# Performance work log

Measured on AMD Instinct MI355X. Metric: run time of the kernel, lower is better.

Reference implementation:

```python
import jax, jax.numpy as jnp
import numpy as np

RADIUS = 0.1      # ball-query radius; also max_dist in collision_error
THRESH = 0.001    # collision threshold
NSAMPLE = 4       # neighbors per query point
EPS = 1e-7
LOSS_WEIGHT = 1.0


def _face_normals(verts, faces):
    # verts: (b, n_v, 3), faces: (b, n_f, 3) int -> unit face normals (b, n_f, 3)
    tri = jax.vmap(lambda V, F: V[F])(verts, faces)  # (b, n_f, 3verts, 3xyz)
    e1 = tri[:, :, 1] - tri[:, :, 0]
    e2 = tri[:, :, 2] - tri[:, :, 0]
    fn = jnp.cross(e1, e2)
    return fn / (jnp.linalg.norm(fn, axis=-1, keepdims=True) + EPS)


def _vertex_normals(faces, fn, n_v):
    # sparse v2f bmm equivalent: average incident face normals per vertex
    def scatter(F, N):
        idx = F.reshape(-1)                    # (3*n_f,) face->vertex ids
        vals = jnp.repeat(N, 3, axis=0)        # each face normal to its 3 verts
        s = jnp.zeros((n_v, 3), N.dtype).at[idx].add(vals)
        c = jnp.zeros((n_v, 1), N.dtype).at[idx].add(jnp.float32(1.0))
        return s / (c + EPS)
    return jax.vmap(scatter)(faces, fn)        # (b, n_v, 3)


def _ball_query(new_xyz, xyz, radius, nsample):
    # PointNet++ ball query: first `nsample` points of xyz within radius of each
    # new_xyz point; unfilled slots repeat the first hit (0 if no hits).
    d2 = jnp.sum((new_xyz[:, :, None, :] - xyz[:, None, :, :]) ** 2, axis=-1)  # (b, nq, nv)
    within = d2 < radius * radius
    c = jnp.cumsum(within.astype(jnp.int32), axis=-1)
    n_within = c[..., -1]
    first_idx = jnp.argmax(within, axis=-1)    # 0 when no hits (matches CUDA kernel)
    slots = []
    for j in range(nsample):
        idx_j = jnp.argmax(within & (c == j + 1), axis=-1)
        slots.append(jnp.where(n_within > j, idx_j, first_idx))
    return jnp.stack(slots, axis=-1)           # (b, nq, nsample)


def _collision_loss(pred, h_state, h_faces):
    faces = jnp.swapaxes(h_faces, 1, 2)                 # (b, n_f, 3)
    human_verts = jnp.swapaxes(h_state, 1, 2)[..., :3]  # (b, n_v, 3)
    n_v = human_verts.shape[1]

    fn = _face_normals(human_verts, faces)
    vn = _vertex_normals(faces, fn, n_v)                # (b, n_v, 3)

    idx = _ball_query(pred, human_verts, RADIUS, NSAMPLE)      # (b, nq, K)
    gxyz = jax.vmap(lambda V, I: V[I])(human_verts, idx)       # (b, nq, K, 3)
    gn = jax.vmap(lambda V, I: V[I])(vn, idx)                  # (b, nq, K, 3)

    diff = pred[:, :, None, :] - gxyz
    gn = gn / (jnp.linalg.norm(gn, axis=-1, keepdims=True) + EPS)
    dot = jnp.sum(diff * gn, axis=-1)                   # (b, nq, K)
    valid_dot = (dot - THRESH) * (dot >= -RADIUS)       # max_dist = radius
    mask = valid_dot < 0
    per_pt = jnp.sum(valid_dot * mask / (jnp.sum(mask, axis=-1, keepdims=True) + EPS), axis=-1) ** 2
    avg_mask = per_pt > 0
    loss = jnp.sum(per_pt)                              # reduction='sum', weight=None
    loss = loss / (jnp.sum(avg_mask) + EPS)
    return LOSS_WEIGHT * loss


def setup_inputs() -> dict:
    key = jax.random.key(0)
    k1, k2, k3, k4 = jax.random.split(key, 4)
    bs, n_pred, n_v, n_f, C = 2, 8192, 6890, 13776, 6
    pred = jax.random.uniform(k1, (bs, n_pred, 3), dtype=jnp.float32)
    label = jax.random.uniform(k2, (bs, n_pred, 3), dtype=jnp.float32)
    h_state = jax.random.uniform(k3, (bs, C, n_v), dtype=jnp.float32)
    h_faces = jax.random.randint(k4, (bs, 3, n_f), 0, n_v, dtype=jnp.int32)
    return {"pred": pred, "label": label, "h_state": h_state, "h_faces": h_faces}


def reference(pred, label, h_state, h_faces):
    # label is unused by collision_error (kept for signature fidelity)
    return _collision_loss(pred, h_state, h_faces)
```

## Files before the change

### kernel.cpp

```cpp
#include <hip/hip_runtime.h>
#include <cstdint>
#include <climits>

#define EPSF 1e-7f
#define NCELL 1000
#define RPAD 0.10002f

__device__ __forceinline__ int cell_of(float x, float y, float z) {
    int cx = min(max((int)(x * 10.0f), 0), 9);
    int cy = min(max((int)(y * 10.0f), 0), 9);
    int cz = min(max((int)(z * 10.0f), 0), 9);
    return (cx * 10 + cy) * 10 + cz;
}

__global__ void k1_face_count(const float* __restrict__ hs,
                              const int* __restrict__ hf,
                              float* __restrict__ svec,
                              float* __restrict__ scnt,
                              int* __restrict__ counts,
                              int n_v, int n_f, int bs) {
    int t = blockIdx.x * blockDim.x + threadIdx.x;
    if (t < bs * n_f) {
        int b = t / n_f;
        int f = t - b * n_f;
        const int* fb = hf + (size_t)b * 3 * n_f;
        int i0 = fb[f];
        int i1 = fb[n_f + f];
        int i2 = fb[2 * n_f + f];
        const float* xs = hs + (size_t)b * 6 * n_v;
        const float* ys = xs + n_v;
        const float* zs = xs + 2 * n_v;
        float ax = xs[i0], ay = ys[i0], az = zs[i0];
        float bx = xs[i1], by = ys[i1], bz = zs[i1];
        float cx = xs[i2], cy = ys[i2], cz = zs[i2];
        float e1x = bx - ax, e1y = by - ay, e1z = bz - az;
        float e2x = cx - ax, e2y = cy - ay, e2z = cz - az;
        float fx = e1y * e2z - e1z * e2y;
        float fy = e1z * e2x - e1x * e2z;
        float fz = e1x * e2y - e1y * e2x;
        float nrm = sqrtf(fx * fx + fy * fy + fz * fz) + EPSF;
        fx /= nrm; fy /= nrm; fz /= nrm;
        float* sb = svec + (size_t)b * n_v * 3;
        float* cb = scnt + (size_t)b * n_v;
        int idx3[3] = {i0, i1, i2};
        #pragma unroll
        for (int k = 0; k < 3; ++k) {
            int i = idx3[k];
            atomicAdd(&sb[i * 3 + 0], fx);
            atomicAdd(&sb[i * 3 + 1], fy);
            atomicAdd(&sb[i * 3 + 2], fz);
            atomicAdd(&cb[i], 1.0f);
        }
    }
    if (t < bs * n_v) {
        int b = t / n_v;
        int v = t - b * n_v;
        const float* xs = hs + (size_t)b * 6 * n_v;
        float x = xs[v], y = xs[n_v + v], z = xs[2 * n_v + v];
        atomicAdd(&counts[b * NCELL + cell_of(x, y, z)], 1);
    }
}

__global__ void k2_vn_scan(float* __restrict__ svec,
                           const float* __restrict__ scnt,
                           const int* __restrict__ counts,
                           int* __restrict__ cellstart,
                           int* __restrict__ cursor,
                           int total_v, int nvb) {
    if (blockIdx.x < (unsigned)nvb) {
        int t = blockIdx.x * blockDim.x + threadIdx.x;
        if (t >= total_v) return;
        float cc = scnt[t] + EPSF;
        float vx = svec[t * 3 + 0] / cc;
        float vy = svec[t * 3 + 1] / cc;
        float vz = svec[t * 3 + 2] / cc;
        float nrm = sqrtf(vx * vx + vy * vy + vz * vz) + EPSF;
        svec[t * 3 + 0] = vx / nrm;
        svec[t * 3 + 1] = vy / nrm;
        svec[t * 3 + 2] = vz / nrm;
        return;
    }
    if (threadIdx.x >= 128) return;
    int batch = threadIdx.x >> 6;
    int lane = threadIdx.x & 63;
    int local[16];
    int mysum = 0;
    #pragma unroll
    for (int k = 0; k < 16; ++k) {
        int c = lane * 16 + k;
        int v = (c < NCELL) ? counts[batch * NCELL + c] : 0;
        local[k] = v;
        mysum += v;
    }
    int s = mysum;
    #pragma unroll
    for (int off = 1; off < 64; off <<= 1) {
        int n = __shfl_up(s, off);
        if (lane >= off) s += n;
    }
    int excl = s - mysum;
    #pragma unroll
    for (int k = 0; k < 16; ++k) {
        int c = lane * 16 + k;
        if (c < NCELL) {
            cellstart[batch * (NCELL + 1) + c] = excl;
            cursor[batch * NCELL + c] = excl;
            excl += local[k];
        }
    }
    if (lane == 63) cellstart[batch * (NCELL + 1) + NCELL] = s;
}

__global__ void k3_scatter(const float* __restrict__ hs,
                           int* __restrict__ cursor,
                           float4* __restrict__ spk,
                           int n_v, int bs) {
    int t = blockIdx.x * blockDim.x + threadIdx.x;
    if (t >= bs * n_v) return;
    int b = t / n_v;
    int v = t - b * n_v;
    const float* xs = hs + (size_t)b * 6 * n_v;
    float x = xs[v], y = xs[n_v + v], z = xs[2 * n_v + v];
    int cell = cell_of(x, y, z);
    int pos = atomicAdd(&cursor[b * NCELL + cell], 1);
    spk[(size_t)b * n_v + pos] = make_float4(x, y, z, __int_as_float(v));
}

__global__ void k4_query(const float* __restrict__ pred,
                         const float* __restrict__ hs,
                         const float* __restrict__ un,
                         const float4* __restrict__ spk,
                         const int* __restrict__ cellstart,
                         double* __restrict__ partial,
                         float* __restrict__ pcnt,
                         int n_v, int n_pred, int bs) {
    const int lane = threadIdx.x & 63;
    const int wave = threadIdx.x >> 6;
    const int wid = blockIdx.x * 4 + wave;
    const int nq = bs * n_pred;

    float per_pt = 0.0f;
    float is_pos = 0.0f;

    if (wid < nq) {
        const int b = wid / n_pred;
        const float* xs = hs + (size_t)b * 6 * n_v;
        const float* ys = xs + n_v;
        const float* zs = xs + 2 * n_v;
        const float* unb = un + (size_t)b * n_v * 3;
        const float4* sp = spk + (size_t)b * n_v;
        const int* csb = cellstart + b * (NCELL + 1);
        const float px = pred[(size_t)wid * 3 + 0];
        const float py = pred[(size_t)wid * 3 + 1];
        const float pz = pred[(size_t)wid * 3 + 2];

        int xlo = max(0, (int)floorf((px - RPAD) * 10.0f));
        int xhi = min(9, (int)floorf((px + RPAD) * 10.0f));
        int ylo = max(0, (int)floorf((py - RPAD) * 10.0f));
        int yhi = min(9, (int)floorf((py + RPAD) * 10.0f));
        int zlo = max(0, (int)floorf((pz - RPAD) * 10.0f));
        int zhi = min(9, (int)floorf((pz + RPAD) * 10.0f));

        int rs[9], re[9];
        #pragma unroll
        for (int i = 0; i < 9; ++i) {
            int cx = xlo + i / 3;
            int cy = ylo + i % 3;
            bool valid = (cx <= xhi) && (cy <= yhi);
            int rowbase = (min(cx, 9) * 10 + min(cy, 9)) * 10;
            int lo = csb[rowbase + zlo];
            int hi = csb[rowbase + zhi + 1];
            rs[i] = valid ? lo : 0;
            re[i] = valid ? hi : 0;
        }

        int l0 = INT_MAX, l1 = INT_MAX, l2 = INT_MAX, l3 = INT_MAX;
        #pragma unroll
        for (int i = 0; i < 9; ++i) {
            for (int p = rs[i] + lane; p < re[i]; p += 64) {
                float4 c4 = sp[p];
                float dx = px - c4.x;
                float dy = py - c4.y;
                float dz = pz - c4.z;
                float d2 = dx * dx + dy * dy + dz * dz;
                if (d2 < 0.01f) {
                    int vid = __float_as_int(c4.w);
                    if (vid < l3) {
                        if (vid < l1) {
                            if (vid < l0) { l3 = l2; l2 = l1; l1 = l0; l0 = vid; }
                            else          { l3 = l2; l2 = l1; l1 = vid; }
                        } else {
                            if (vid < l2) { l3 = l2; l2 = vid; }
                            else          { l3 = vid; }
                        }
                    }
                }
            }
        }

        int a0 = l0, a1 = l1, a2 = l2, a3 = l3;
        int s0, s1, s2, s3;
        #pragma unroll
        for (int j = 0; j < 4; ++j) {
            int m = a0;
            #pragma unroll
            for (int off = 1; off < 64; off <<= 1) m = min(m, __shfl_xor(m, off));
            if (j == 0) s0 = m; else if (j == 1) s1 = m; else if (j == 2) s2 = m; else s3 = m;
            if (a0 == m && m != INT_MAX) { a0 = a1; a1 = a2; a2 = a3; a3 = INT_MAX; }
        }
        int id0 = (s0 == INT_MAX) ? 0 : s0;
        int id1 = (s1 == INT_MAX) ? id0 : s1;
        int id2 = (s2 == INT_MAX) ? id0 : s2;
        int id3 = (s3 == INT_MAX) ? id0 : s3;
        int ids[4] = {id0, id1, id2, id3};

        float vd[4];
        float cm = 0.0f;
        #pragma unroll
        for (int j = 0; j < 4; ++j) {
            int id = ids[j];
            float dx = px - xs[id];
            float dy = py - ys[id];
            float dz = pz - zs[id];
            float nx = unb[id * 3 + 0];
            float ny = unb[id * 3 + 1];
            float nz = unb[id * 3 + 2];
            float dot = dx * nx + dy * ny + dz * nz;
            float w = (dot >= -0.1f) ? 1.0f : 0.0f;
            float v = (dot - 0.001f) * w;
            bool msk = v < 0.0f;
            vd[j] = msk ? v : 0.0f;
            cm += msk ? 1.0f : 0.0f;
        }
        float s = ((vd[0] + vd[1]) + vd[2]) + vd[3];
        float a = s / (cm + EPSF);
        per_pt = a * a;
        is_pos = (per_pt > 0.0f) ? 1.0f : 0.0f;
    }

    __shared__ float ls[4];
    __shared__ float lc[4];
    if (lane == 0) { ls[wave] = per_pt; lc[wave] = is_pos; }
    __syncthreads();
    if (threadIdx.x == 0) {
        partial[blockIdx.x] = (double)ls[0] + (double)ls[1] + (double)ls[2] + (double)ls[3];
        pcnt[blockIdx.x] = ((lc[0] + lc[1]) + lc[2]) + lc[3];
    }
}

__global__ void finalize_kernel(const double* __restrict__ partial,
                                const float* __restrict__ pcnt,
                                int n, float* __restrict__ out) {
    double s = 0.0, c = 0.0;
    for (int i = threadIdx.x; i < n; i += blockDim.x) {
        s += partial[i];
        c += (double)pcnt[i];
    }
    #pragma unroll
    for (int off = 32; off > 0; off >>= 1) {
        s += __shfl_down(s, off);
        c += __shfl_down(c, off);
    }
    __shared__ double ws_s[4];
    __shared__ double ws_c[4];
    int wave = threadIdx.x >> 6;
    int lane = threadIdx.x & 63;
    if (lane == 0) { ws_s[wave] = s; ws_c[wave] = c; }
    __syncthreads();
    if (threadIdx.x == 0) {
        double S = ws_s[0] + ws_s[1] + ws_s[2] + ws_s[3];
        double C = ws_c[0] + ws_c[1] + ws_c[2] + ws_c[3];
        out[0] = (float)(S / (C + 1e-7));
    }
}

extern "C" void kernel_launch(void* const* d_in, const int* in_sizes, int n_in,
                              void* d_out, int out_size, void* d_ws, size_t ws_size,
                              hipStream_t stream) {
    const float* pred    = (const float*)d_in[0];
    const float* h_state = (const float*)d_in[2];
    const int*   h_faces = (const int*)d_in[3];
    float* out = (float*)d_out;

    const int bs = 2;
    const int n_pred = in_sizes[0] / (bs * 3);
    const int n_v    = in_sizes[2] / (bs * 6);
    const int n_f    = in_sizes[3] / (bs * 3);
    const int nq = bs * n_pred;
    const int nblk = (nq + 3) / 4;

    size_t o_svec    = 0;
    size_t o_scnt    = o_svec + (size_t)bs * n_v * 3;
    size_t o_counts  = o_scnt + (size_t)bs * n_v;
    size_t o_zeroend = (o_counts + (size_t)bs * NCELL + 3) & ~(size_t)3;
    size_t o_cursor  = o_zeroend;
    size_t o_cs      = o_cursor + (size_t)bs * NCELL;
    size_t o_partial = (o_cs + (size_t)bs * (NCELL + 1) + 1) & ~(size_t)1;
    size_t o_pcnt    = o_partial + 2 * (size_t)nblk;
    size_t o_spk     = (o_pcnt + (size_t)nblk + 3) & ~(size_t)3;

    float* base = (float*)d_ws;
    float*  svec      = base + o_svec;
    float*  scnt      = base + o_scnt;
    int*    counts    = (int*)(base + o_counts);
    int*    cursor    = (int*)(base + o_cursor);
    int*    cellstart = (int*)(base + o_cs);
    double* partial   = (double*)(base + o_partial);
    float*  pcnt      = base + o_pcnt;
    float4* spk       = (float4*)(base + o_spk);

    hipMemsetAsync(d_ws, 0, o_zeroend * sizeof(float), stream);

    int t1 = bs * n_f;
    k1_face_count<<<(t1 + 255) / 256, 256, 0, stream>>>(
        h_state, h_faces, svec, scnt, counts, n_v, n_f, bs);

    int nvb = (bs * n_v + 255) / 256;
    k2_vn_scan<<<nvb + 1, 256, 0, stream>>>(
        svec, scnt, counts, cellstart, cursor, bs * n_v, nvb);

    k3_scatter<<<(bs * n_v + 255) / 256, 256, 0, stream>>>(
        h_state, cursor, spk, n_v, bs);

    k4_query<<<nblk, 256, 0, stream>>>(
        pred, h_state, svec, spk, cellstart, partial, pcnt,
        n_v, n_pred, bs);

    finalize_kernel<<<1, 256, 0, stream>>>(partial, pcnt, nblk, out);
}
```

Baseline: 111.2 us.

## Fuse scan and scatter into one kernel, flatten cell loop, pack vertex data

The prefix scan and the vertex scatter are merged into one kernel that uses a shared-memory cursor per batch, and one launch is dropped. The query kernel flattens its nine per-row cell loops into a single index space and prefetches up to six float4 groups before computing distances, to raise memory-level parallelism. The four rounds of wave min-reduction are replaced by a butterfly merge of sorted top-4 lists. Vertex positions and normals are packed as float4 pairs for the final gather. The scatter now runs on only one block per batch, which serialises that work, and the fixed candidate prefetch buffer raises register pressure.

```diff
diff --git a/kernel.cpp b/kernel.cpp
--- a/kernel.cpp
+++ b/kernel.cpp
@@ -5,6 +5,7 @@
 #define EPSF 1e-7f
 #define NCELL 1000
 #define RPAD 0.10002f
+#define MAXG 6
 
 __device__ __forceinline__ int cell_of(float x, float y, float z) {
     int cx = min(max((int)(x * 10.0f), 0), 9);
@@ -61,74 +62,73 @@
     }
 }
 
-__global__ void k2_vn_scan(float* __restrict__ svec,
-                           const float* __restrict__ scnt,
-                           const int* __restrict__ counts,
-                           int* __restrict__ cellstart,
-                           int* __restrict__ cursor,
-                           int total_v, int nvb) {
+__global__ void k2_build(const float* __restrict__ hs,
+                         const float* __restrict__ svec,
+                         const float* __restrict__ scnt,
+                         const int* __restrict__ counts,
+                         int* __restrict__ cellstart,
+                         float4* __restrict__ vert,
+                         float4* __restrict__ spk,
+                         int n_v, int bs, int nvb) {
+    __shared__ int cursor_l[NCELL];
     if (blockIdx.x < (unsigned)nvb) {
         int t = blockIdx.x * blockDim.x + threadIdx.x;
-        if (t >= total_v) return;
+        if (t >= bs * n_v) return;
+        int b = t / n_v;
+        int v = t - b * n_v;
         float cc = scnt[t] + EPSF;
         float vx = svec[t * 3 + 0] / cc;
         float vy = svec[t * 3 + 1] / cc;
         float vz = svec[t * 3 + 2] / cc;
         float nrm = sqrtf(vx * vx + vy * vy + vz * vz) + EPSF;
-        svec[t * 3 + 0] = vx / nrm;
-        svec[t * 3 + 1] = vy / nrm;
-        svec[t * 3 + 2] = vz / nrm;
+        const float* xs = hs + (size_t)b * 6 * n_v;
+        float x = xs[v], y = xs[n_v + v], z = xs[2 * n_v + v];
+        vert[2 * (size_t)t + 0] = make_float4(x, y, z, 0.0f);
+        vert[2 * (size_t)t + 1] = make_float4(vx / nrm, vy / nrm, vz / nrm, 0.0f);
         return;
     }
-    if (threadIdx.x >= 128) return;
-    int batch = threadIdx.x >> 6;
-    int lane = threadIdx.x & 63;
-    int local[16];
-    int mysum = 0;
-    #pragma unroll
-    for (int k = 0; k < 16; ++k) {
-        int c = lane * 16 + k;
-        int v = (c < NCELL) ? counts[batch * NCELL + c] : 0;
-        local[k] = v;
-        mysum += v;
-    }
-    int s = mysum;
-    #pragma unroll
-    for (int off = 1; off < 64; off <<= 1) {
-        int n = __shfl_up(s, off);
-        if (lane >= off) s += n;
-    }
-    int excl = s - mysum;
-    #pragma unroll
-    for (int k = 0; k < 16; ++k) {
-        int c = lane * 16 + k;
-        if (c < NCELL) {
-            cellstart[batch * (NCELL + 1) + c] = excl;
-            cursor[batch * NCELL + c] = excl;
-            excl += local[k];
-        }
-    }
-    if (lane == 63) cellstart[batch * (NCELL + 1) + NCELL] = s;
-}
-
-__global__ void k3_scatter(const float* __restrict__ hs,
-                           int* __restrict__ cursor,
-                           float4* __restrict__ spk,
-                           int n_v, int bs) {
-    int t = blockIdx.x * blockDim.x + threadIdx.x;
-    if (t >= bs * n_v) return;
-    int b = t / n_v;
-    int v = t - b * n_v;
-    const float* xs = hs + (size_t)b * 6 * n_v;
-    float x = xs[v], y = xs[n_v + v], z = xs[2 * n_v + v];
-    int cell = cell_of(x, y, z);
-    int pos = atomicAdd(&cursor[b * NCELL + cell], 1);
-    spk[(size_t)b * n_v + pos] = make_float4(x, y, z, __int_as_float(v));
-}
-
-__global__ void k4_query(const float* __restrict__ pred,
-                         const float* __restrict__ hs,
-                         const float* __restrict__ un,
+    int batch = blockIdx.x - nvb;
+    if (threadIdx.x < 64) {
+        int lane = threadIdx.x;
+        int local[16];
+        int mysum = 0;
+        #pragma unroll
+        for (int k = 0; k < 16; ++k) {
+            int c = lane * 16 + k;
+            int v = (c < NCELL) ? counts[batch * NCELL + c] : 0;
+            local[k] = v;
+            mysum += v;
+        }
+        int s = mysum;
+        #pragma unroll
+        for (int off = 1; off < 64; off <<= 1) {
+            int n = __shfl_up(s, off);
+            if (lane >= off) s += n;
+        }
+        int excl = s - mysum;
+        #pragma unroll
+        for (int k = 0; k < 16; ++k) {
+            int c = lane * 16 + k;
+            if (c < NCELL) {
+                cellstart[batch * (NCELL + 1) + c] = excl;
+                cursor_l[c] = excl;
+                excl += local[k];
+            }
+        }
+        if (lane == 63) cellstart[batch * (NCELL + 1) + NCELL] = s;
+    }
+    __syncthreads();
+    const float* xs = hs + (size_t)batch * 6 * n_v;
+    for (int v = threadIdx.x; v < n_v; v += blockDim.x) {
+        float x = xs[v], y = xs[n_v + v], z = xs[2 * n_v + v];
+        int cell = cell_of(x, y, z);
+        int pos = atomicAdd(&cursor_l[cell], 1);
+        spk[(size_t)batch * n_v + pos] = make_float4(x, y, z, __int_as_float(v));
+    }
+}
+
+__global__ void k3_query(const float* __restrict__ pred,
+                         const float4* __restrict__ vert,
                          const float4* __restrict__ spk,
                          const int* __restrict__ cellstart,
                          double* __restrict__ partial,
@@ -144,10 +144,7 @@
 
     if (wid < nq) {
         const int b = wid / n_pred;
-        const float* xs = hs + (size_t)b * 6 * n_v;
-        const float* ys = xs + n_v;
-        const float* zs = xs + 2 * n_v;
-        const float* unb = un + (size_t)b * n_v * 3;
+        const float4* vb = vert + 2 * (size_t)b * n_v;
         const float4* sp = spk + (size_t)b * n_v;
         const int* csb = cellstart + b * (NCELL + 1);
         const float px = pred[(size_t)wid * 3 + 0];
@@ -173,12 +170,61 @@
             rs[i] = valid ? lo : 0;
             re[i] = valid ? hi : 0;
         }
+        int B[10];
+        B[0] = 0;
+        #pragma unroll
+        for (int i = 0; i < 9; ++i) B[i + 1] = B[i] + (re[i] - rs[i]);
+        const int T = B[9];
+        int D[9];
+        #pragma unroll
+        for (int i = 0; i < 9; ++i) D[i] = rs[i] - B[i];
 
         int l0 = INT_MAX, l1 = INT_MAX, l2 = INT_MAX, l3 = INT_MAX;
-        #pragma unroll
-        for (int i = 0; i < 9; ++i) {
-            for (int p = rs[i] + lane; p < re[i]; p += 64) {
-                float4 c4 = sp[p];
+
+        if (T > 0) {
+            float4 cbuf[MAXG];
+            #pragma unroll
+            for (int g = 0; g < MAXG; ++g) {
+                if (g * 64 < T) {
+                    int pc = min(g * 64 + lane, T - 1);
+                    int addr = pc + D[0];
+                    #pragma unroll
+                    for (int i = 1; i < 9; ++i)
+                        addr = (pc >= B[i]) ? pc + D[i] : addr;
+                    cbuf[g] = sp[addr];
+                }
+            }
+            #pragma unroll
+            for (int g = 0; g < MAXG; ++g) {
+                if (g * 64 < T) {
+                    int p = g * 64 + lane;
+                    if (p < T) {
+                        float4 c4 = cbuf[g];
+                        float dx = px - c4.x;
+                        float dy = py - c4.y;
+                        float dz = pz - c4.z;
+                        float d2 = dx * dx + dy * dy + dz * dz;
+                        if (d2 < 0.01f) {
+                            int vid = __float_as_int(c4.w);
+                            if (vid < l3) {
+                                if (vid < l1) {
+                                    if (vid < l0) { l3 = l2; l2 = l1; l1 = l0; l0 = vid; }
+                                    else          { l3 = l2; l2 = l1; l1 = vid; }
+                                } else {
+                                    if (vid < l2) { l3 = l2; l2 = vid; }
+                                    else          { l3 = vid; }
+                                }
+                            }
+                        }
+                    }
+                }
+            }
+            for (int p = MAXG * 64 + lane; p < T; p += 64) {
+                int addr = p + D[0];
+                #pragma unroll
+                for (int i = 1; i < 9; ++i)
+                    addr = (p >= B[i]) ? p + D[i] : addr;
+                float4 c4 = sp[addr];
                 float dx = px - c4.x;
                 float dy = py - c4.y;
                 float dz = pz - c4.z;
@@ -198,20 +244,26 @@
             }
         }
 
-        int a0 = l0, a1 = l1, a2 = l2, a3 = l3;
-        int s0, s1, s2, s3;
-        #pragma unroll
-        for (int j = 0; j < 4; ++j) {
-            int m = a0;
-            #pragma unroll
-            for (int off = 1; off < 64; off <<= 1) m = min(m, __shfl_xor(m, off));
-            if (j == 0) s0 = m; else if (j == 1) s1 = m; else if (j == 2) s2 = m; else s3 = m;
-            if (a0 == m && m != INT_MAX) { a0 = a1; a1 = a2; a2 = a3; a3 = INT_MAX; }
-        }
-        int id0 = (s0 == INT_MAX) ? 0 : s0;
-        int id1 = (s1 == INT_MAX) ? id0 : s1;
-        int id2 = (s2 == INT_MAX) ? id0 : s2;
-        int id3 = (s3 == INT_MAX) ? id0 : s3;
+        #pragma unroll
+        for (int off = 1; off < 64; off <<= 1) {
+            int r0 = __shfl_xor(l3, off);
+            int r1 = __shfl_xor(l2, off);
+            int r2 = __shfl_xor(l1, off);
+            int r3 = __shfl_xor(l0, off);
+            int m0 = min(l0, r0);
+            int m1 = min(l1, r1);
+            int m2 = min(l2, r2);
+            int m3 = min(l3, r3);
+            int t0 = min(m0, m2), t2 = max(m0, m2);
+            int t1 = min(m1, m3), t3 = max(m1, m3);
+            l0 = min(t0, t1); l1 = max(t0, t1);
+            l2 = min(t2, t3); l3 = max(t2, t3);
+        }
+
+        int id0 = (l0 == INT_MAX) ? 0 : l0;
+        int id1 = (l1 == INT_MAX) ? id0 : l1;
+        int id2 = (l2 == INT_MAX) ? id0 : l2;
+        int id3 = (l3 == INT_MAX) ? id0 : l3;
         int ids[4] = {id0, id1, id2, id3};
 
         float vd[4];
@@ -219,13 +271,12 @@
         #pragma unroll
         for (int j = 0; j < 4; ++j) {
             int id = ids[j];
-            float dx = px - xs[id];
-            float dy = py - ys[id];
-            float dz = pz - zs[id];
-            float nx = unb[id * 3 + 0];
-            float ny = unb[id * 3 + 1];
-            float nz = unb[id * 3 + 2];
-            float dot = dx * nx + dy * ny + dz * nz;
+            float4 cj = vb[2 * id + 0];
+            float4 nj = vb[2 * id + 1];
+            float dx = px - cj.x;
+            float dy = py - cj.y;
+            float dz = pz - cj.z;
+            float dot = dx * nj.x + dy * nj.y + dz * nj.z;
             float w = (dot >= -0.1f) ? 1.0f : 0.0f;
             float v = (dot - 0.001f) * w;
             bool msk = v < 0.0f;
@@ -293,21 +344,21 @@
     size_t o_scnt    = o_svec + (size_t)bs * n_v * 3;
     size_t o_counts  = o_scnt + (size_t)bs * n_v;
     size_t o_zeroend = (o_counts + (size_t)bs * NCELL + 3) & ~(size_t)3;
-    size_t o_cursor  = o_zeroend;
-    size_t o_cs      = o_cursor + (size_t)bs * NCELL;
+    size_t o_cs      = o_zeroend;
     size_t o_partial = (o_cs + (size_t)bs * (NCELL + 1) + 1) & ~(size_t)1;
     size_t o_pcnt    = o_partial + 2 * (size_t)nblk;
     size_t o_spk     = (o_pcnt + (size_t)nblk + 3) & ~(size_t)3;
+    size_t o_vert    = o_spk + (size_t)bs * n_v * 4;
 
     float* base = (float*)d_ws;
     float*  svec      = base + o_svec;
     float*  scnt      = base + o_scnt;
     int*    counts    = (int*)(base + o_counts);
-    int*    cursor    = (int*)(base + o_cursor);
     int*    cellstart = (int*)(base + o_cs);
     double* partial   = (double*)(base + o_partial);
     float*  pcnt      = base + o_pcnt;
     float4* spk       = (float4*)(base + o_spk);
+    float4* vert      = (float4*)(base + o_vert);
 
     hipMemsetAsync(d_ws, 0, o_zeroend * sizeof(float), stream);
 
@@ -316,15 +367,11 @@
         h_state, h_faces, svec, scnt, counts, n_v, n_f, bs);
 
     int nvb = (bs * n_v + 255) / 256;
-    k2_vn_scan<<<nvb + 1, 256, 0, stream>>>(
-        svec, scnt, counts, cellstart, cursor, bs * n_v, nvb);
-
-    k3_scatter<<<(bs * n_v + 255) / 256, 256, 0, stream>>>(
-        h_state, cursor, spk, n_v, bs);
-
-    k4_query<<<nblk, 256, 0, stream>>>(
-        pred, h_state, svec, spk, cellstart, partial, pcnt,
-        n_v, n_pred, bs);
+    k2_build<<<nvb + bs, 256, 0, stream>>>(
+        h_state, svec, scnt, counts, cellstart, vert, spk, n_v, bs, nvb);
+
+    k3_query<<<nblk, 256, 0, stream>>>(
+        pred, vert, spk, cellstart, partial, pcnt, n_v, n_pred, bs);
 
     finalize_kernel<<<1, 256, 0, stream>>>(partial, pcnt, nblk, out);
 }
```

After: 113.6 us. 2.1% more time.
